# Optimization experiments

Measured on AMD Instinct MI355X. Metric: run time of the kernel, lower is better.

## Reference

```python
import jax, jax.numpy as jnp
import numpy as np

N = 500_000
E = 8_000_000
F = 16


def setup_inputs() -> dict:
    key = jax.random.key(0)
    ks = jax.random.split(key, 8)
    x = jax.random.normal(ks[0], (N, F), dtype=jnp.float32)
    h0 = jax.random.normal(ks[1], (N, F), dtype=jnp.float32)
    adj_row = jnp.sort(jax.random.randint(ks[2], (E,), 0, N, dtype=jnp.int32)).astype(jnp.int64)
    adj_col = jax.random.randint(ks[3], (E,), 0, N, dtype=jnp.int32).astype(jnp.int64)
    adj_val = jax.random.uniform(ks[4], (E,), dtype=jnp.float32)
    stdv = 1.0 / np.sqrt(F)
    weight = jax.random.uniform(ks[5], (2 * F, F), minval=-stdv, maxval=stdv, dtype=jnp.float32)
    fc_w = jax.random.normal(ks[6], (1, F), dtype=jnp.float32) * 0.1
    fc_b = jax.random.normal(ks[7], (1,), dtype=jnp.float32) * 0.1
    lamda = jnp.ones((1,), dtype=jnp.float32) * 0.5
    l = 2
    return {"x": x, "h0": h0, "adj_row": adj_row, "adj_col": adj_col,
            "adj_val": adj_val, "weight": weight, "fc_w": fc_w, "fc_b": fc_b,
            "lamda": lamda, "l": l}


def reference(x, h0, adj_row, adj_col, adj_val, weight, fc_w, fc_b, lamda, l):
    n = x.shape[0]
    # sparse aggregation: hi = A @ x  (COO spmm via gather + segment_sum)
    hi = jax.ops.segment_sum(adj_val[:, None] * x[adj_col], adj_row, num_segments=n)  # [N, F]
    # small MLP gate: alpha = Linear(16,1)(hi)
    alpha = hi @ fc_w.T + fc_b  # [N, 1]
    theta = jnp.log(lamda / l + 1.0)  # [1], broadcasts
    support = jnp.concatenate([hi, h0], axis=1)  # [N, 2F] (variant=True)
    r = (1.0 - alpha) * hi + alpha * h0  # [N, F]
    out = theta * (support @ weight) + (1.0 - theta) * r
    return out + x  # residual=True
```

## Files before the change

### kernel.cpp

```cpp
#include <hip/hip_runtime.h>

#define FDIM 16
#define RPB  16
#define CAP  1024

__global__ __launch_bounds__(256) void rowptr_kernel(const int* __restrict__ rows,
                                                     int* __restrict__ row_ptr,
                                                     long long nedge, int n) {
  long long e = (long long)blockIdx.x * blockDim.x + threadIdx.x;
  if (e >= nedge) return;
  int b = rows[e];
  if (e == 0) {
    for (int r = 0; r <= b; ++r) row_ptr[r] = 0;
  } else {
    int a = rows[e - 1];
    for (int r = a + 1; r <= b; ++r) row_ptr[r] = (int)e;
  }
  if (e == nedge - 1) {
    for (int r = b + 1; r <= n; ++r) row_ptr[r] = (int)nedge;
  }
}

__global__ __launch_bounds__(256) void spmm_fuse_kernel(
    const int* __restrict__ row_ptr,
    const int* __restrict__ cols,
    const float* __restrict__ vals,
    const float* __restrict__ x,
    const float* __restrict__ h0,
    const float* __restrict__ weight,
    const float* __restrict__ fc_w,
    const float* __restrict__ fc_b,
    const float* __restrict__ lamda,
    const int* __restrict__ lpar,
    float* __restrict__ out,
    int n) {
  __shared__ float wsh[2 * FDIM * FDIM];
  __shared__ int   lc[CAP];
  __shared__ float lv[CAP];
  for (int i = threadIdx.x; i < 2 * FDIM * FDIM; i += blockDim.x)
    wsh[i] = weight[i];

  int g = threadIdx.x >> 4;
  int f = threadIdx.x & 15;
  int R0 = blockIdx.x * RPB;
  int r = R0 + g;
  int Rend = min(R0 + RPB, n);

  int s_blk = row_ptr[R0];
  int t_blk = row_ptr[Rend];
  int s_g = 0, t_g = 0;
  if (r < n) { s_g = row_ptr[r]; t_g = row_ptr[r + 1]; }

  float acc = 0.f;
  for (int t0 = s_blk; t0 < t_blk; t0 += CAP) {
    int t1 = min(t0 + CAP, t_blk);
    __syncthreads();
    for (int i = t0 + (int)threadIdx.x; i < t1; i += 256) {
      lc[i - t0] = cols[i];
      lv[i - t0] = vals[i];
    }
    __syncthreads();

    int a = max(s_g, t0), b = min(t_g, t1);
    int e = a;
    for (; e + 8 <= b; e += 8) {
      int j = e - t0;
      int   c0 = lc[j + 0], c1 = lc[j + 1], c2 = lc[j + 2], c3 = lc[j + 3];
      int   c4 = lc[j + 4], c5 = lc[j + 5], c6 = lc[j + 6], c7 = lc[j + 7];
      float v0 = lv[j + 0], v1 = lv[j + 1], v2 = lv[j + 2], v3 = lv[j + 3];
      float v4 = lv[j + 4], v5 = lv[j + 5], v6 = lv[j + 6], v7 = lv[j + 7];
      float g0 = x[c0 * FDIM + f], g1 = x[c1 * FDIM + f];
      float g2 = x[c2 * FDIM + f], g3 = x[c3 * FDIM + f];
      float g4 = x[c4 * FDIM + f], g5 = x[c5 * FDIM + f];
      float g6 = x[c6 * FDIM + f], g7 = x[c7 * FDIM + f];
      acc = fmaf(v0, g0, acc); acc = fmaf(v1, g1, acc);
      acc = fmaf(v2, g2, acc); acc = fmaf(v3, g3, acc);
      acc = fmaf(v4, g4, acc); acc = fmaf(v5, g5, acc);
      acc = fmaf(v6, g6, acc); acc = fmaf(v7, g7, acc);
    }
    if (e + 4 <= b) {
      int j = e - t0;
      int   c0 = lc[j + 0], c1 = lc[j + 1], c2 = lc[j + 2], c3 = lc[j + 3];
      float v0 = lv[j + 0], v1 = lv[j + 1], v2 = lv[j + 2], v3 = lv[j + 3];
      float g0 = x[c0 * FDIM + f], g1 = x[c1 * FDIM + f];
      float g2 = x[c2 * FDIM + f], g3 = x[c3 * FDIM + f];
      acc = fmaf(v0, g0, acc); acc = fmaf(v1, g1, acc);
      acc = fmaf(v2, g2, acc); acc = fmaf(v3, g3, acc);
      e += 4;
    }
    for (; e < b; ++e)
      acc = fmaf(lv[e - t0], x[lc[e - t0] * FDIM + f], acc);
  }
  __syncthreads();

  if (r >= n) return;

  float h0f = h0[(size_t)r * FDIM + f];
  float xf  = x[(size_t)r * FDIM + f];
  float theta = logf(lamda[0] / (float)lpar[0] + 1.0f);

  float av = acc * fc_w[f];
  av += __shfl_xor(av, 1, 16);
  av += __shfl_xor(av, 2, 16);
  av += __shfl_xor(av, 4, 16);
  av += __shfl_xor(av, 8, 16);
  float alpha = av + fc_b[0];

  float sf = 0.f;
#pragma unroll
  for (int k = 0; k < FDIM; ++k) {
    float hk  = __shfl(acc, k, 16);
    float h0k = __shfl(h0f, k, 16);
    sf = fmaf(hk,  wsh[k * FDIM + f], sf);
    sf = fmaf(h0k, wsh[(FDIM + k) * FDIM + f], sf);
  }

  float rr = (1.f - alpha) * acc + alpha * h0f;
  out[(size_t)r * FDIM + f] = fmaf(theta, sf, (1.f - theta) * rr) + xf;
}

extern "C" void kernel_launch(void* const* d_in, const int* in_sizes, int n_in,
                              void* d_out, int out_size, void* d_ws, size_t ws_size,
                              hipStream_t stream) {
  const float* x        = (const float*)d_in[0];
  const float* h0       = (const float*)d_in[1];
  const int* adj_row    = (const int*)d_in[2];
  const int* adj_col    = (const int*)d_in[3];
  const float* adj_val  = (const float*)d_in[4];
  const float* weight   = (const float*)d_in[5];
  const float* fc_w     = (const float*)d_in[6];
  const float* fc_b     = (const float*)d_in[7];
  const float* lamda    = (const float*)d_in[8];
  const int* lpar       = (const int*)d_in[9];

  int n = in_sizes[0] / FDIM;
  long long nedge = in_sizes[2];
  float* out = (float*)d_out;
  int* row_ptr = (int*)d_ws;

  long long rb = (nedge + 255) / 256;
  rowptr_kernel<<<(int)rb, 256, 0, stream>>>(adj_row, row_ptr, nedge, n);

  int sb = (n + RPB - 1) / RPB;
  spmm_fuse_kernel<<<sb, 256, 0, stream>>>(row_ptr, adj_col, adj_val, x, h0,
                                           weight, fc_w, fc_b, lamda, lpar,
                                           out, n);
}
```

Before: 171.8 us.

## Balance SpMM edges across thread groups with segmented shared-memory atomic accumulation

Splits each block's edge chunk evenly across 32 groups of 8 threads, so work no longer follows per-row edge counts. Each group keeps running sums and flushes them with shared-memory atomics into a per-row accumulator whenever the row index changes. Each thread now gathers float2 from x instead of a scalar, and the block covers 32 rows instead of 16. This removes load imbalance from uneven row lengths and halves the number of gather instructions. In exchange it reads adj_row again, adds LDS atomics, and adds an extra barrier per chunk.

```diff
diff --git a/kernel.cpp b/kernel.cpp
--- a/kernel.cpp
+++ b/kernel.cpp
@@ -1,7 +1,8 @@
 #include <hip/hip_runtime.h>
 
 #define FDIM 16
-#define RPB  16
+#define RPB  32
+#define NG   32
 #define CAP  1024
 
 __global__ __launch_bounds__(256) void rowptr_kernel(const int* __restrict__ rows,
@@ -23,6 +24,7 @@
 
 __global__ __launch_bounds__(256) void spmm_fuse_kernel(
     const int* __restrict__ row_ptr,
+    const int* __restrict__ rows,
     const int* __restrict__ cols,
     const float* __restrict__ vals,
     const float* __restrict__ x,
@@ -35,88 +37,131 @@
     float* __restrict__ out,
     int n) {
   __shared__ float wsh[2 * FDIM * FDIM];
+  __shared__ int   lr[CAP];
   __shared__ int   lc[CAP];
   __shared__ float lv[CAP];
-  for (int i = threadIdx.x; i < 2 * FDIM * FDIM; i += blockDim.x)
-    wsh[i] = weight[i];
+  __shared__ float lhi[RPB][FDIM];
 
-  int g = threadIdx.x >> 4;
-  int f = threadIdx.x & 15;
+  int tid = (int)threadIdx.x;
+  for (int i = tid; i < 2 * FDIM * FDIM; i += 256) wsh[i] = weight[i];
+  for (int i = tid; i < RPB * FDIM; i += 256) ((float*)lhi)[i] = 0.f;
+
+  int g = tid >> 3;
+  int l = tid & 7;
   int R0 = blockIdx.x * RPB;
+  int Rend = min(R0 + RPB, n);
   int r = R0 + g;
-  int Rend = min(R0 + RPB, n);
 
   int s_blk = row_ptr[R0];
   int t_blk = row_ptr[Rend];
-  int s_g = 0, t_g = 0;
-  if (r < n) { s_g = row_ptr[r]; t_g = row_ptr[r + 1]; }
 
-  float acc = 0.f;
+  __syncthreads();
+
+  const float2* __restrict__ x2 = reinterpret_cast<const float2*>(x);
+
   for (int t0 = s_blk; t0 < t_blk; t0 += CAP) {
     int t1 = min(t0 + CAP, t_blk);
-    __syncthreads();
-    for (int i = t0 + (int)threadIdx.x; i < t1; i += 256) {
-      lc[i - t0] = cols[i];
-      lv[i - t0] = vals[i];
+    int len = t1 - t0;
+    for (int i = tid; i < len; i += 256) {
+      lr[i] = rows[t0 + i] - R0;
+      lc[i] = cols[t0 + i];
+      lv[i] = vals[t0 + i];
     }
     __syncthreads();
 
-    int a = max(s_g, t0), b = min(t_g, t1);
-    int e = a;
-    for (; e + 8 <= b; e += 8) {
-      int j = e - t0;
-      int   c0 = lc[j + 0], c1 = lc[j + 1], c2 = lc[j + 2], c3 = lc[j + 3];
-      int   c4 = lc[j + 4], c5 = lc[j + 5], c6 = lc[j + 6], c7 = lc[j + 7];
-      float v0 = lv[j + 0], v1 = lv[j + 1], v2 = lv[j + 2], v3 = lv[j + 3];
-      float v4 = lv[j + 4], v5 = lv[j + 5], v6 = lv[j + 6], v7 = lv[j + 7];
-      float g0 = x[c0 * FDIM + f], g1 = x[c1 * FDIM + f];
-      float g2 = x[c2 * FDIM + f], g3 = x[c3 * FDIM + f];
-      float g4 = x[c4 * FDIM + f], g5 = x[c5 * FDIM + f];
-      float g6 = x[c6 * FDIM + f], g7 = x[c7 * FDIM + f];
-      acc = fmaf(v0, g0, acc); acc = fmaf(v1, g1, acc);
-      acc = fmaf(v2, g2, acc); acc = fmaf(v3, g3, acc);
-      acc = fmaf(v4, g4, acc); acc = fmaf(v5, g5, acc);
-      acc = fmaf(v6, g6, acc); acc = fmaf(v7, g7, acc);
+    int a = (len * g) >> 5;
+    int b = (len * (g + 1)) >> 5;
+    if (a < b) {
+      int cur = lr[a];
+      float ax = 0.f, ay = 0.f;
+
+#define FLUSH()                                   \
+      { atomicAdd(&lhi[cur][2 * l],     ax);      \
+        atomicAdd(&lhi[cur][2 * l + 1], ay);      \
+        ax = 0.f; ay = 0.f; }
+#define STEP(r_, v_, gx_, gy_)                    \
+      if (r_ != cur) { FLUSH(); cur = r_; }       \
+      ax = fmaf(v_, gx_, ax);                     \
+      ay = fmaf(v_, gy_, ay);
+
+      int e = a;
+      for (; e + 8 <= b; e += 8) {
+        int   r0 = lr[e+0], r1 = lr[e+1], r2 = lr[e+2], r3 = lr[e+3];
+        int   r4 = lr[e+4], r5 = lr[e+5], r6 = lr[e+6], r7 = lr[e+7];
+        int   c0 = lc[e+0], c1 = lc[e+1], c2 = lc[e+2], c3 = lc[e+3];
+        int   c4 = lc[e+4], c5 = lc[e+5], c6 = lc[e+6], c7 = lc[e+7];
+        float v0 = lv[e+0], v1 = lv[e+1], v2 = lv[e+2], v3 = lv[e+3];
+        float v4 = lv[e+4], v5 = lv[e+5], v6 = lv[e+6], v7 = lv[e+7];
+        float2 g0 = x2[c0 * 8 + l], g1 = x2[c1 * 8 + l];
+        float2 g2 = x2[c2 * 8 + l], g3 = x2[c3 * 8 + l];
+        float2 g4 = x2[c4 * 8 + l], g5 = x2[c5 * 8 + l];
+        float2 g6 = x2[c6 * 8 + l], g7 = x2[c7 * 8 + l];
+        if (r7 == cur) {
+          ax = fmaf(v0, g0.x, ax); ay = fmaf(v0, g0.y, ay);
+          ax = fmaf(v1, g1.x, ax); ay = fmaf(v1, g1.y, ay);
+          ax = fmaf(v2, g2.x, ax); ay = fmaf(v2, g2.y, ay);
+          ax = fmaf(v3, g3.x, ax); ay = fmaf(v3, g3.y, ay);
+          ax = fmaf(v4, g4.x, ax); ay = fmaf(v4, g4.y, ay);
+          ax = fmaf(v5, g5.x, ax); ay = fmaf(v5, g5.y, ay);
+          ax = fmaf(v6, g6.x, ax); ay = fmaf(v6, g6.y, ay);
+          ax = fmaf(v7, g7.x, ax); ay = fmaf(v7, g7.y, ay);
+        } else {
+          STEP(r0, v0, g0.x, g0.y)
+          STEP(r1, v1, g1.x, g1.y)
+          STEP(r2, v2, g2.x, g2.y)
+          STEP(r3, v3, g3.x, g3.y)
+          STEP(r4, v4, g4.x, g4.y)
+          STEP(r5, v5, g5.x, g5.y)
+          STEP(r6, v6, g6.x, g6.y)
+          STEP(r7, v7, g7.x, g7.y)
+        }
+      }
+      for (; e < b; ++e) {
+        int rr_ = lr[e];
+        float2 gg = x2[lc[e] * 8 + l];
+        STEP(rr_, lv[e], gg.x, gg.y)
+      }
+      FLUSH();
+#undef STEP
+#undef FLUSH
     }
-    if (e + 4 <= b) {
-      int j = e - t0;
-      int   c0 = lc[j + 0], c1 = lc[j + 1], c2 = lc[j + 2], c3 = lc[j + 3];
-      float v0 = lv[j + 0], v1 = lv[j + 1], v2 = lv[j + 2], v3 = lv[j + 3];
-      float g0 = x[c0 * FDIM + f], g1 = x[c1 * FDIM + f];
-      float g2 = x[c2 * FDIM + f], g3 = x[c3 * FDIM + f];
-      acc = fmaf(v0, g0, acc); acc = fmaf(v1, g1, acc);
-      acc = fmaf(v2, g2, acc); acc = fmaf(v3, g3, acc);
-      e += 4;
-    }
-    for (; e < b; ++e)
-      acc = fmaf(lv[e - t0], x[lc[e - t0] * FDIM + f], acc);
+    __syncthreads();
   }
+
   __syncthreads();
 
   if (r >= n) return;
 
-  float h0f = h0[(size_t)r * FDIM + f];
-  float xf  = x[(size_t)r * FDIM + f];
+  float2 hi2 = make_float2(lhi[g][2 * l], lhi[g][2 * l + 1]);
+  float2 h02 = reinterpret_cast<const float2*>(h0)[(size_t)r * 8 + l];
+  float2 xf2 = reinterpret_cast<const float2*>(x)[(size_t)r * 8 + l];
   float theta = logf(lamda[0] / (float)lpar[0] + 1.0f);
 
-  float av = acc * fc_w[f];
-  av += __shfl_xor(av, 1, 16);
-  av += __shfl_xor(av, 2, 16);
-  av += __shfl_xor(av, 4, 16);
-  av += __shfl_xor(av, 8, 16);
+  float av = hi2.x * fc_w[2 * l] + hi2.y * fc_w[2 * l + 1];
+  av += __shfl_xor(av, 1, 8);
+  av += __shfl_xor(av, 2, 8);
+  av += __shfl_xor(av, 4, 8);
   float alpha = av + fc_b[0];
 
-  float sf = 0.f;
+  const float2* wsh2 = reinterpret_cast<const float2*>(wsh);
+  float sx = 0.f, sy = 0.f;
 #pragma unroll
   for (int k = 0; k < FDIM; ++k) {
-    float hk  = __shfl(acc, k, 16);
-    float h0k = __shfl(h0f, k, 16);
-    sf = fmaf(hk,  wsh[k * FDIM + f], sf);
-    sf = fmaf(h0k, wsh[(FDIM + k) * FDIM + f], sf);
+    float hk  = lhi[g][k];
+    float h0k = (k & 1) ? __shfl(h02.y, k >> 1, 8)
+                        : __shfl(h02.x, k >> 1, 8);
+    float2 w1 = wsh2[k * 8 + l];
+    float2 w2 = wsh2[(FDIM + k) * 8 + l];
+    sx = fmaf(hk, w1.x, sx);  sy = fmaf(hk, w1.y, sy);
+    sx = fmaf(h0k, w2.x, sx); sy = fmaf(h0k, w2.y, sy);
   }
 
-  float rr = (1.f - alpha) * acc + alpha * h0f;
-  out[(size_t)r * FDIM + f] = fmaf(theta, sf, (1.f - theta) * rr) + xf;
+  float rx = (1.f - alpha) * hi2.x + alpha * h02.x;
+  float ry = (1.f - alpha) * hi2.y + alpha * h02.y;
+  float2 o;
+  o.x = fmaf(theta, sx, (1.f - theta) * rx) + xf2.x;
+  o.y = fmaf(theta, sy, (1.f - theta) * ry) + xf2.y;
+  reinterpret_cast<float2*>(out)[(size_t)r * 8 + l] = o;
 }
 
 extern "C" void kernel_launch(void* const* d_in, const int* in_sizes, int n_in,
@@ -142,7 +187,7 @@
   rowptr_kernel<<<(int)rb, 256, 0, stream>>>(adj_row, row_ptr, nedge, n);
 
   int sb = (n + RPB - 1) / RPB;
-  spmm_fuse_kernel<<<sb, 256, 0, stream>>>(row_ptr, adj_col, adj_val, x, h0,
-                                           weight, fc_w, fc_b, lamda, lpar,
-                                           out, n);
+  spmm_fuse_kernel<<<sb, 256, 0, stream>>>(row_ptr, adj_row, adj_col, adj_val,
+                                           x, h0, weight, fc_w, fc_b, lamda,
+                                           lpar, out, n);
 }
```

New measurement: 174.5 us. Within noise of the previous version (+1.5%).
